# Performance work log

Hardware: AMD Instinct MI355X
Metric: run time of the kernel (lower is better)

Reference implementation:

```python
import jax, jax.numpy as jnp
import numpy as np

T = 2048   # timesteps
S = 512    # state_len (MMD buffer length)
D = 128    # latent_dim


def setup_inputs() -> dict:
    key = jax.random.key(0)
    k1, k2 = jax.random.split(key)
    x = jax.random.normal(k1, (1, T, 1, D), dtype=jnp.float32)
    initial_state = jax.random.normal(k2, (S, D), dtype=jnp.float32)
    return {"x": x, "initial_state": initial_state}


def reference(x, initial_state):
    # x: [1, T, 1, D]; initial_state: [S, D]
    latent_dim = x.shape[-1]
    z_seq = x[0, :, 0, :]  # [T, D] -- batch=1 stream, as the TF module assumes

    def step(d, z):
        # d: [S, D] shifting buffer of past latents; z: [D] current latent
        # polynomial kernel: (1 - ||z - d_i||^2 / latent_dim)^3 for each buffer row
        gamma = (-1.0 / latent_dim) * jnp.sum((z[None, :] - d) ** 2, axis=-1)  # [S]
        poly = (1.0 + gamma) ** 3                                              # [S]
        # shift buffer: newest latent in front, drop oldest
        d_new = jnp.concatenate([z[None, :], d[:-1]], axis=0)                  # [S, D]
        return d_new, poly

    _, kernel = jax.lax.scan(step, initial_state, z_seq)  # kernel: [T, S]
    return kernel[None, :, :]  # [1, T, S] == K.rnn outputs with batch=1
```

## Files before the change

kernel.cpp:

```cpp
#include <hip/hip_runtime.h>

#define T_LEN 2048
#define S_LEN 512
#define D_LEN 128
#define BT 64
#define BG 64


__global__ __launch_bounds__(256, 2)
void mmd_kernel(const float* __restrict__ x, const float* __restrict__ init,
                float* __restrict__ out) {
    __shared__ float zt[BT * D_LEN];
    __shared__ float gt[BG * D_LEN];
    __shared__ float znorm[BT];
    __shared__ float gnorm[BG];

    const int bt = blockIdx.y;
    const int j  = blockIdx.x;
    const int t0 = bt * BT;
    const int g0 = t0 + j * 64;

    const int tid = threadIdx.x;

    for (int idx = tid; idx < BT * 32; idx += 256) {
        const int row = idx >> 5;
        const int c4  = idx & 31;
        const float4 v = *(const float4*)(x + (t0 + row) * D_LEN + c4 * 4);
        *(float4*)(zt + row * D_LEN + ((c4 ^ (row & 7)) << 2)) = v;
    }
    for (int idx = tid; idx < BG * 32; idx += 256) {
        const int row = idx >> 5;
        const int c4  = idx & 31;
        const int g = g0 + row;
        const float* src = (g >= S_LEN) ? (x + (g - S_LEN) * D_LEN)
                                        : (init + (S_LEN - 1 - g) * D_LEN);
        const float4 v = *(const float4*)(src + c4 * 4);
        *(float4*)(gt + row * D_LEN + ((c4 ^ (row & 7)) << 2)) = v;
    }
    __syncthreads();

    if (tid < 128) {
        const int row = tid & 63;
        const float* base = (tid < 64) ? zt : gt;
        float s = 0.f;
        #pragma unroll 8
        for (int c4 = 0; c4 < 32; ++c4) {
            const float4 v = *(const float4*)(base + row * D_LEN + ((c4 ^ (row & 7)) << 2));
            s += v.x * v.x + v.y * v.y + v.z * v.z + v.w * v.w;
        }
        if (tid < 64) znorm[row] = s; else gnorm[row] = s;
    }
    __syncthreads();

    const int tx = tid & 15;
    const int ty = tid >> 4;

    float dot[4][4];
    #pragma unroll
    for (int i = 0; i < 4; ++i)
        #pragma unroll
        for (int jj = 0; jj < 4; ++jj) dot[i][jj] = 0.f;

    #pragma unroll 4
    for (int k4 = 0; k4 < 32; ++k4) {
        float4 za[4], wb[4];
        #pragma unroll
        for (int i = 0; i < 4; ++i) {
            const int row = i * 16 + ty;
            za[i] = *(const float4*)(zt + row * D_LEN + ((k4 ^ (row & 7)) << 2));
        }
        #pragma unroll
        for (int jj = 0; jj < 4; ++jj) {
            const int row = jj * 16 + tx;
            wb[jj] = *(const float4*)(gt + row * D_LEN + ((k4 ^ (row & 7)) << 2));
        }
        #pragma unroll
        for (int i = 0; i < 4; ++i) {
            #pragma unroll
            for (int jj = 0; jj < 4; ++jj) {
                dot[i][jj] += za[i].x * wb[jj].x + za[i].y * wb[jj].y
                            + za[i].z * wb[jj].z + za[i].w * wb[jj].w;
            }
        }
    }

    #pragma unroll
    for (int i = 0; i < 4; ++i) {
        const int tr = i * 16 + ty;
        const int t  = t0 + tr;
        #pragma unroll
        for (int jj = 0; jj < 4; ++jj) {
            const int gr = jj * 16 + tx;
            const int g  = g0 + gr;
            const int s  = t + (S_LEN - 1) - g;
            if (s >= 0 && s < S_LEN) {
                const float dist = znorm[tr] + gnorm[gr] - 2.f * dot[i][jj];
                const float p = 1.f - dist * (1.f / (float)D_LEN);
                out[t * S_LEN + s] = p * p * p;
            }
        }
    }
}

extern "C" void kernel_launch(void* const* d_in, const int* in_sizes, int n_in,
                              void* d_out, int out_size, void* d_ws, size_t ws_size,
                              hipStream_t stream) {
    const float* x    = (const float*)d_in[0];
    const float* init = (const float*)d_in[1];
    float* out = (float*)d_out;

    dim3 grid(9, 32);
    mmd_kernel<<<grid, 256, 0, stream>>>(x, init, out);
}
```

Baseline: 70.27 us.

## Compute buffer dot products with split-bf16 MFMA and retile to 64x80 blocks

Replaces the scalar FP32 dot-product loop with MFMA 16x16x32 bf16 instructions. Each FP32 value is split into a high and a low bf16 part, and three MFMAs per tile keep close to FP32 accuracy. Norms are now computed during the load with wave shuffles instead of a separate pass and barrier. Tiles change to 64x80 with 512 threads and an 8x32 grid, which cuts the redundant edge blocks. The risk is precision loss from the 3-term bf16 split, plus extra conversion work at load time.

```diff
diff --git a/kernel.cpp b/kernel.cpp
--- a/kernel.cpp
+++ b/kernel.cpp
@@ -4,99 +4,153 @@
 #define S_LEN 512
 #define D_LEN 128
 #define BT 64
-#define BG 64
+#define BG 80
+#define THREADS 512
 
 
-__global__ __launch_bounds__(256, 2)
+typedef __attribute__((ext_vector_type(8))) short short8;
+typedef __attribute__((ext_vector_type(4))) float f32x4;
+
+__device__ __forceinline__ unsigned int bf16_rne(float f) {
+    unsigned int u = __float_as_uint(f);
+    u += 0x7FFFu + ((u >> 16) & 1u);
+    return u >> 16;
+}
+
+__global__ __launch_bounds__(THREADS, 2)
 void mmd_kernel(const float* __restrict__ x, const float* __restrict__ init,
                 float* __restrict__ out) {
-    __shared__ float zt[BT * D_LEN];
-    __shared__ float gt[BG * D_LEN];
+    __shared__ uint4 zh4[BT * 16];
+    __shared__ uint4 zl4[BT * 16];
+    __shared__ uint4 gh4[BG * 16];
+    __shared__ uint4 gl4[BG * 16];
     __shared__ float znorm[BT];
     __shared__ float gnorm[BG];
 
-    const int bt = blockIdx.y;
-    const int j  = blockIdx.x;
-    const int t0 = bt * BT;
-    const int g0 = t0 + j * 64;
-
+    const int t0 = blockIdx.y * BT;
+    const int g0 = t0 + blockIdx.x * BG;
     const int tid = threadIdx.x;
 
-    for (int idx = tid; idx < BT * 32; idx += 256) {
-        const int row = idx >> 5;
-        const int c4  = idx & 31;
-        const float4 v = *(const float4*)(x + (t0 + row) * D_LEN + c4 * 4);
-        *(float4*)(zt + row * D_LEN + ((c4 ^ (row & 7)) << 2)) = v;
+    #pragma unroll
+    for (int k = 0; k < 2; ++k) {
+        const int idx = tid + k * THREADS;
+        const int row = idx >> 4;
+        const int c   = idx & 15;
+        const float* p = x + (t0 + row) * D_LEN + c * 8;
+        const float4 va = *(const float4*)p;
+        const float4 vb = *(const float4*)(p + 4);
+        const float f[8] = {va.x, va.y, va.z, va.w, vb.x, vb.y, vb.z, vb.w};
+        unsigned int h[8], l[8];
+        float nrm = 0.f;
+        #pragma unroll
+        for (int e = 0; e < 8; ++e) {
+            nrm += f[e] * f[e];
+            h[e] = bf16_rne(f[e]);
+            const float fh = __uint_as_float(h[e] << 16);
+            l[e] = bf16_rne(f[e] - fh);
+        }
+        uint4 H, L;
+        H.x = h[0] | (h[1] << 16); H.y = h[2] | (h[3] << 16);
+        H.z = h[4] | (h[5] << 16); H.w = h[6] | (h[7] << 16);
+        L.x = l[0] | (l[1] << 16); L.y = l[2] | (l[3] << 16);
+        L.z = l[4] | (l[5] << 16); L.w = l[6] | (l[7] << 16);
+        const int slot = c ^ (row & 15);
+        zh4[row * 16 + slot] = H;
+        zl4[row * 16 + slot] = L;
+        nrm += __shfl_xor(nrm, 1);
+        nrm += __shfl_xor(nrm, 2);
+        nrm += __shfl_xor(nrm, 4);
+        nrm += __shfl_xor(nrm, 8);
+        if (c == 0) znorm[row] = nrm;
     }
-    for (int idx = tid; idx < BG * 32; idx += 256) {
-        const int row = idx >> 5;
-        const int c4  = idx & 31;
-        const int g = g0 + row;
-        const float* src = (g >= S_LEN) ? (x + (g - S_LEN) * D_LEN)
-                                        : (init + (S_LEN - 1 - g) * D_LEN);
-        const float4 v = *(const float4*)(src + c4 * 4);
-        *(float4*)(gt + row * D_LEN + ((c4 ^ (row & 7)) << 2)) = v;
+    #pragma unroll
+    for (int k = 0; k < 3; ++k) {
+        const int idx = tid + k * THREADS;
+        if (idx < BG * 16) {
+            const int row = idx >> 4;
+            const int c   = idx & 15;
+            int g = g0 + row;
+            if (g > T_LEN + S_LEN - 1) g = T_LEN + S_LEN - 1;
+            const float* src = (g >= S_LEN) ? (x + (g - S_LEN) * D_LEN)
+                                            : (init + (S_LEN - 1 - g) * D_LEN);
+            const float4 va = *(const float4*)(src + c * 8);
+            const float4 vb = *(const float4*)(src + c * 8 + 4);
+            const float f[8] = {va.x, va.y, va.z, va.w, vb.x, vb.y, vb.z, vb.w};
+            unsigned int h[8], l[8];
+            float nrm = 0.f;
+            #pragma unroll
+            for (int e = 0; e < 8; ++e) {
+                nrm += f[e] * f[e];
+                h[e] = bf16_rne(f[e]);
+                const float fh = __uint_as_float(h[e] << 16);
+                l[e] = bf16_rne(f[e] - fh);
+            }
+            uint4 H, L;
+            H.x = h[0] | (h[1] << 16); H.y = h[2] | (h[3] << 16);
+            H.z = h[4] | (h[5] << 16); H.w = h[6] | (h[7] << 16);
+            L.x = l[0] | (l[1] << 16); L.y = l[2] | (l[3] << 16);
+            L.z = l[4] | (l[5] << 16); L.w = l[6] | (l[7] << 16);
+            const int slot = c ^ (row & 15);
+            gh4[row * 16 + slot] = H;
+            gl4[row * 16 + slot] = L;
+            nrm += __shfl_xor(nrm, 1);
+            nrm += __shfl_xor(nrm, 2);
+            nrm += __shfl_xor(nrm, 4);
+            nrm += __shfl_xor(nrm, 8);
+            if (c == 0) gnorm[row] = nrm;
+        }
     }
     __syncthreads();
 
-    if (tid < 128) {
-        const int row = tid & 63;
-        const float* base = (tid < 64) ? zt : gt;
-        float s = 0.f;
-        #pragma unroll 8
-        for (int c4 = 0; c4 < 32; ++c4) {
-            const float4 v = *(const float4*)(base + row * D_LEN + ((c4 ^ (row & 7)) << 2));
-            s += v.x * v.x + v.y * v.y + v.z * v.z + v.w * v.w;
-        }
-        if (tid < 64) znorm[row] = s; else gnorm[row] = s;
-    }
-    __syncthreads();
+    const int lane = tid & 63;
+    const int wid  = tid >> 6;
+    const int r16  = lane & 15;
+    const int g4   = lane >> 4;
+    const int R    = wid >> 1;
+    const int half = wid & 1;
+    const int cb   = half ? 3 : 0;
+    const int nt   = half ? 2 : 3;
 
-    const int tx = tid & 15;
-    const int ty = tid >> 4;
+    f32x4 acc[3];
+    #pragma unroll
+    for (int ti = 0; ti < 3; ++ti) acc[ti] = (f32x4){0.f, 0.f, 0.f, 0.f};
 
-    float dot[4][4];
+    const int arow = R * 16 + r16;
+
     #pragma unroll
-    for (int i = 0; i < 4; ++i)
+    for (int q = 0; q < 4; ++q) {
+        const int slot = (q * 4 + g4) ^ r16;
+        const short8 Ah = *(const short8*)(zh4 + arow * 16 + slot);
+        const short8 Al = *(const short8*)(zl4 + arow * 16 + slot);
         #pragma unroll
-        for (int jj = 0; jj < 4; ++jj) dot[i][jj] = 0.f;
-
-    #pragma unroll 4
-    for (int k4 = 0; k4 < 32; ++k4) {
-        float4 za[4], wb[4];
-        #pragma unroll
-        for (int i = 0; i < 4; ++i) {
-            const int row = i * 16 + ty;
-            za[i] = *(const float4*)(zt + row * D_LEN + ((k4 ^ (row & 7)) << 2));
-        }
-        #pragma unroll
-        for (int jj = 0; jj < 4; ++jj) {
-            const int row = jj * 16 + tx;
-            wb[jj] = *(const float4*)(gt + row * D_LEN + ((k4 ^ (row & 7)) << 2));
-        }
-        #pragma unroll
-        for (int i = 0; i < 4; ++i) {
-            #pragma unroll
-            for (int jj = 0; jj < 4; ++jj) {
-                dot[i][jj] += za[i].x * wb[jj].x + za[i].y * wb[jj].y
-                            + za[i].z * wb[jj].z + za[i].w * wb[jj].w;
+        for (int ti = 0; ti < 3; ++ti) {
+            if (ti < nt) {
+                const int gi = ((cb + ti) * 16 + r16) * 16 + slot;
+                const short8 Bh = *(const short8*)(gh4 + gi);
+                const short8 Bl = *(const short8*)(gl4 + gi);
+                acc[ti] = __builtin_amdgcn_mfma_f32_16x16x32_bf16(Ah, Bh, acc[ti], 0, 0, 0);
+                acc[ti] = __builtin_amdgcn_mfma_f32_16x16x32_bf16(Ah, Bl, acc[ti], 0, 0, 0);
+                acc[ti] = __builtin_amdgcn_mfma_f32_16x16x32_bf16(Al, Bh, acc[ti], 0, 0, 0);
             }
         }
     }
 
     #pragma unroll
-    for (int i = 0; i < 4; ++i) {
-        const int tr = i * 16 + ty;
-        const int t  = t0 + tr;
-        #pragma unroll
-        for (int jj = 0; jj < 4; ++jj) {
-            const int gr = jj * 16 + tx;
+    for (int ti = 0; ti < 3; ++ti) {
+        if (ti < nt) {
+            const int gr = (cb + ti) * 16 + r16;
             const int g  = g0 + gr;
-            const int s  = t + (S_LEN - 1) - g;
-            if (s >= 0 && s < S_LEN) {
-                const float dist = znorm[tr] + gnorm[gr] - 2.f * dot[i][jj];
-                const float p = 1.f - dist * (1.f / (float)D_LEN);
-                out[t * S_LEN + s] = p * p * p;
+            const float gn = gnorm[gr];
+            #pragma unroll
+            for (int reg = 0; reg < 4; ++reg) {
+                const int row = R * 16 + g4 * 4 + reg;
+                const int t   = t0 + row;
+                const int s   = t + (S_LEN - 1) - g;
+                if (s >= 0 && s < S_LEN) {
+                    const float dist = znorm[row] + gn - 2.f * acc[ti][reg];
+                    const float p = 1.f - dist * (1.f / (float)D_LEN);
+                    out[t * S_LEN + s] = p * p * p;
+                }
             }
         }
     }
@@ -105,10 +159,11 @@
 extern "C" void kernel_launch(void* const* d_in, const int* in_sizes, int n_in,
                               void* d_out, int out_size, void* d_ws, size_t ws_size,
                               hipStream_t stream) {
+    (void)in_sizes; (void)n_in; (void)out_size; (void)d_ws; (void)ws_size;
     const float* x    = (const float*)d_in[0];
     const float* init = (const float*)d_in[1];
     float* out = (float*)d_out;
 
-    dim3 grid(9, 32);
-    mmd_kernel<<<grid, 256, 0, stream>>>(x, init, out);
+    dim3 grid(8, 32);
+    mmd_kernel<<<grid, THREADS, 0, stream>>>(x, init, out);
 }
```

After: 60.63 us. -13.7%, faster.
